# Optimization experiments

Hardware: AMD Instinct MI355X
Metric: run time of the kernel (lower is better)

Reference implementation:

```python
import jax, jax.numpy as jnp
import numpy as np
from math import lgamma, pi, sqrt

L = 20  # legendre_polys; embedding_dim = L*L = 400
SQ2 = sqrt(2.0)

def _norm(l, m):
    # K(l,m) = sqrt((2l+1)/(4pi) * (l-m)!/(l+m)!), computed stably via lgamma
    return sqrt((2 * l + 1) / (4.0 * pi)) * sqrt(np.exp(lgamma(l - m + 1) - lgamma(l + m + 1)))

def setup_inputs() -> dict:
    key = jax.random.key(0)
    k1, k2 = jax.random.split(key)
    B = 250000
    lon = jax.random.uniform(k1, (B,), minval=-180.0, maxval=180.0)
    lat = jax.random.uniform(k2, (B,), minval=-90.0, maxval=90.0)
    return {"lonlat": jnp.stack([lon, lat], axis=-1).astype(jnp.float32)}

def _sh_all(lonlat):
    # Real spherical harmonics for all (l, m), l in [0, L), m in [-l, l],
    # in the same ordering as the torch module's double loop.
    lon, lat = lonlat[:, 0], lonlat[:, 1]
    phi = jnp.deg2rad(lon + 180.0)    # azimuth in [0, 2pi)
    theta = jnp.deg2rad(lat + 90.0)   # colatitude in [0, pi]
    x = jnp.cos(theta)
    sx = jnp.sin(theta)               # = sqrt(1 - x^2) on [0, pi]

    # Associated Legendre P_l^m(x) (Condon-Shortley phase) via recurrence.
    P = {(0, 0): jnp.ones_like(x)}
    for m in range(1, L):
        P[(m, m)] = -(2 * m - 1) * sx * P[(m - 1, m - 1)]
    for m in range(L):
        if m + 1 < L:
            P[(m + 1, m)] = (2 * m + 1) * x * P[(m, m)]
        for l in range(m + 2, L):
            P[(l, m)] = ((2 * l - 1) * x * P[(l - 1, m)] - (l + m - 1) * P[(l - 2, m)]) / (l - m)

    cols = []
    for l in range(L):
        for m in range(-l, l + 1):
            am = abs(m)
            K = _norm(l, am)
            if m > 0:
                cols.append(SQ2 * K * jnp.cos(m * phi) * P[(l, m)])
            elif m < 0:
                cols.append(SQ2 * K * jnp.sin(am * phi) * P[(l, am)])
            else:
                cols.append(K * P[(l, 0)])
    return jnp.stack(cols, axis=-1)  # [B, L*L]

def reference(lonlat):
    return _sh_all(lonlat)
```

## Files before the change

kernel.cpp:

```cpp
#include <hip/hip_runtime.h>


#define L_MAX 20
#define NCOL 400
#define PTS 64
#define TPB 256
#define LSTR 205
#define SPLIT_L 14
#define C0A 0
#define CA 196
#define C0B 196
#define CB 204

constexpr double csqrt(double x) {
    double g = (x > 1.0) ? x : 1.0;
    for (int i = 0; i < 200; ++i) g = 0.5 * (g + x / g);
    return g;
}

struct CoefTbl { float c[NCOL]; };

constexpr CoefTbl make_tbl() {
    CoefTbl t{};
    const double PI  = 3.14159265358979323846;
    const double SQ2 = csqrt(2.0);
    for (int l = 0; l < L_MAX; ++l) {
        for (int m = 0; m <= l; ++m) {
            double r = 1.0;
            for (int k = l - m + 1; k <= l + m; ++k) r /= (double)k;
            double K = csqrt((2.0 * l + 1.0) / (4.0 * PI) * r);
            int base = l * l + l;
            if (m == 0) {
                t.c[base] = (float)K;
            } else {
                t.c[base + m] = (float)(SQ2 * K);
                t.c[base - m] = (float)(SQ2 * K);
            }
        }
    }
    return t;
}

static constexpr CoefTbl TBL = make_tbl();

__device__ constexpr int SUBOF[L_MAX] =
    {0,1,2,3, 3,2,1,0, 0,1,2,3, 3,2, 1,0,0,1, 2,3};

template<int L0, int L1, int C0>
__device__ __forceinline__ void sh_pass(int sub, float x, float sx,
                                        float c1, float s1,
                                        float* __restrict__ myrow) {
    constexpr int LTOP = L1 - 1;
    float pm = 1.0f;
    float cv = 1.0f, sv = 0.0f;

    auto emit = [&](int l, int m, float p) {
        if (l < L0) return;
        const int g = l * l + l;
        const int b = g - C0;
        if (m == 0) {
            myrow[b] = TBL.c[g] * p;
        } else {
            const float t = TBL.c[g + m] * p;
            myrow[b + m] = t * cv;
            myrow[b - m] = t * sv;
        }
    };

#pragma unroll
    for (int m = 0; m <= LTOP; ++m) {
        if (SUBOF[m] == sub) {
            float p2 = pm;
            emit(m, m, p2);
            if (m + 1 <= LTOP) {
                float p1 = float(2 * m + 1) * x * p2;
                emit(m + 1, m, p1);
#pragma unroll
                for (int l = m + 2; l <= LTOP; ++l) {
                    float p0 = (float(2 * l - 1) * x * p1 -
                                float(l + m - 1) * p2) *
                               (1.0f / float(l - m));
                    emit(l, m, p0);
                    p2 = p1; p1 = p0;
                }
            }
        }
        if (m < LTOP) {
            pm = -float(2 * m + 1) * sx * pm;
            float cn = cv * c1 - sv * s1;
            sv = sv * c1 + cv * s1;
            cv = cn;
        }
    }
}

template<int C0, int CW>
__device__ __forceinline__ void flush(const float* __restrict__ tile,
                                      float* __restrict__ outBase,
                                      int tid, int rem) {
    constexpr int G = CW / 4;
    constexpr int N = PTS * G;
    if (rem >= PTS) {
#pragma unroll 4
        for (int i = tid; i < N; i += TPB) {
            int pp = i / G;
            int cc = (i - pp * G) * 4;
            const float* s = tile + pp * LSTR + cc;
            float4 v = make_float4(s[0], s[1], s[2], s[3]);
            *reinterpret_cast<float4*>(outBase + pp * NCOL + C0 + cc) = v;
        }
    } else {
        for (int i = tid; i < N; i += TPB) {
            int pp = i / G;
            int cc = (i - pp * G) * 4;
            if (pp < rem) {
                const float* s = tile + pp * LSTR + cc;
                float4 v = make_float4(s[0], s[1], s[2], s[3]);
                *reinterpret_cast<float4*>(outBase + pp * NCOL + C0 + cc) = v;
            }
        }
    }
}

__global__ __launch_bounds__(TPB, 3) void sh_kernel(const float2* __restrict__ lonlat,
                                                    float* __restrict__ out, int B) {
    __shared__ float tile[PTS * LSTR];

    const int tid  = threadIdx.x;
    const int lane = tid & 63;
    const int sub  = tid >> 6;
    const int blockBase = blockIdx.x * PTS;
    const int rem = B - blockBase;
    const int p  = blockBase + lane;
    const int pr = p < B ? p : B - 1;

    float2 ll = lonlat[pr];
    const float D2R = 0.017453292519943295f;
    float phi   = (ll.x + 180.0f) * D2R;
    float theta = (ll.y + 90.0f) * D2R;

    float x, sx, s1, c1;
    sincosf(theta, &sx, &x);
    sincosf(phi, &s1, &c1);

    float* myrow = tile + lane * LSTR;
    float* outBase = out + (size_t)blockBase * NCOL;

    sh_pass<0, SPLIT_L, C0A>(sub, x, sx, c1, s1, myrow);

    __syncthreads();
    flush<C0A, CA>(tile, outBase, tid, rem);
    __syncthreads();

    sh_pass<SPLIT_L, L_MAX, C0B>(sub, x, sx, c1, s1, myrow);

    __syncthreads();
    flush<C0B, CB>(tile, outBase, tid, rem);
}

extern "C" void kernel_launch(void* const* d_in, const int* in_sizes, int n_in,
                              void* d_out, int out_size, void* d_ws, size_t ws_size,
                              hipStream_t stream) {
    (void)n_in; (void)d_ws; (void)ws_size; (void)out_size;
    const float2* lonlat = (const float2*)d_in[0];
    float* out = (float*)d_out;
    int B = in_sizes[0] / 2;

    const int blocks = (B + PTS - 1) / PTS;
    sh_kernel<<<blocks, TPB, 0, stream>>>(lonlat, out, B);
}
```

Measured before the change: 446.0 us.

## Double-buffer LDS tile across seven l-chunks, overlapping flush with compute

Restructures the kernel from two compute/flush phases into seven l-range chunks. Each chunk keeps its Legendre recurrence state in registers across chunks and writes into one of two smaller ping-pong LDS buffers, so one chunk's global store overlaps the next chunk's computation. It also replaces __syncthreads with a raw s_barrier plus an lgkmcnt wait, drops one barrier per stage, and raises the occupancy hint from 3 to 4. The cost is more barriers in total, more live registers for the per-m recurrence state, and narrower flush widths with more loop overhead.

Measured after the change: 463.5 us. +3.9%, slower.

```diff
diff --git a/kernel.cpp b/kernel.cpp
--- a/kernel.cpp
+++ b/kernel.cpp
@@ -5,12 +5,7 @@
 #define NCOL 400
 #define PTS 64
 #define TPB 256
-#define LSTR 205
-#define SPLIT_L 14
-#define C0A 0
-#define CA 196
-#define C0B 196
-#define CB 204
+#define LSTR 77
 
 constexpr double csqrt(double x) {
     double g = (x > 1.0) ? x : 1.0;
@@ -46,66 +41,61 @@
 __device__ constexpr int SUBOF[L_MAX] =
     {0,1,2,3, 3,2,1,0, 0,1,2,3, 3,2, 1,0,0,1, 2,3};
 
+#define BARRIER() do {                                      \
+    asm volatile("s_waitcnt lgkmcnt(0)" ::: "memory");      \
+    __builtin_amdgcn_s_barrier();                           \
+    asm volatile("" ::: "memory");                          \
+} while (0)
+
 template<int L0, int L1, int C0>
-__device__ __forceinline__ void sh_pass(int sub, float x, float sx,
-                                        float c1, float s1,
-                                        float* __restrict__ myrow) {
-    constexpr int LTOP = L1 - 1;
-    float pm = 1.0f;
-    float cv = 1.0f, sv = 0.0f;
-
-    auto emit = [&](int l, int m, float p) {
-        if (l < L0) return;
+__device__ __forceinline__ void computeChunk(int sub, float x,
+        float (&p1)[5], float (&p2)[5], const float (&pmmv)[5],
+        const float (&cmv)[5], const float (&smv)[5],
+        float* __restrict__ myrow) {
+#pragma unroll
+    for (int l = L0; l < L1; ++l) {
         const int g = l * l + l;
-        const int b = g - C0;
-        if (m == 0) {
-            myrow[b] = TBL.c[g] * p;
-        } else {
-            const float t = TBL.c[g + m] * p;
-            myrow[b + m] = t * cv;
-            myrow[b - m] = t * sv;
-        }
-    };
-
-#pragma unroll
-    for (int m = 0; m <= LTOP; ++m) {
-        if (SUBOF[m] == sub) {
-            float p2 = pm;
-            emit(m, m, p2);
-            if (m + 1 <= LTOP) {
-                float p1 = float(2 * m + 1) * x * p2;
-                emit(m + 1, m, p1);
-#pragma unroll
-                for (int l = m + 2; l <= LTOP; ++l) {
-                    float p0 = (float(2 * l - 1) * x * p1 -
-                                float(l + m - 1) * p2) *
-                               (1.0f / float(l - m));
-                    emit(l, m, p0);
-                    p2 = p1; p1 = p0;
-                }
-            }
-        }
-        if (m < LTOP) {
-            pm = -float(2 * m + 1) * sx * pm;
-            float cn = cv * c1 - sv * s1;
-            sv = sv * c1 + cv * s1;
-            cv = cn;
-        }
-    }
-}
-
-template<int C0, int CW>
-__device__ __forceinline__ void flush(const float* __restrict__ tile,
-                                      float* __restrict__ outBase,
-                                      int tid, int rem) {
-    constexpr int G = CW / 4;
+#pragma unroll
+        for (int m = 0; m <= l; ++m) {
+            if (SUBOF[m] != sub) continue;
+            const int s = m >> 2;
+            float pv;
+            if (l == m) {
+                pv = pmmv[s];
+                p1[s] = pv;
+            } else if (l == m + 1) {
+                pv = float(2 * m + 1) * x * p1[s];
+                p2[s] = p1[s];
+                p1[s] = pv;
+            } else {
+                pv = (float(2 * l - 1) * x * p1[s] -
+                      float(l + m - 1) * p2[s]) * (1.0f / float(l - m));
+                p2[s] = p1[s];
+                p1[s] = pv;
+            }
+            const int b = g - C0;
+            if (m == 0) {
+                myrow[b] = TBL.c[g] * pv;
+            } else {
+                const float t = TBL.c[g + m] * pv;
+                myrow[b + m] = t * cmv[s];
+                myrow[b - m] = t * smv[s];
+            }
+        }
+    }
+}
+
+template<int C0, int W>
+__device__ __forceinline__ void flushChunk(const float* __restrict__ src,
+                                           float* __restrict__ outBase,
+                                           int tid, int rem) {
+    constexpr int G = W / 4;
     constexpr int N = PTS * G;
     if (rem >= PTS) {
-#pragma unroll 4
         for (int i = tid; i < N; i += TPB) {
             int pp = i / G;
             int cc = (i - pp * G) * 4;
-            const float* s = tile + pp * LSTR + cc;
+            const float* s = src + pp * LSTR + cc;
             float4 v = make_float4(s[0], s[1], s[2], s[3]);
             *reinterpret_cast<float4*>(outBase + pp * NCOL + C0 + cc) = v;
         }
@@ -114,7 +104,7 @@
             int pp = i / G;
             int cc = (i - pp * G) * 4;
             if (pp < rem) {
-                const float* s = tile + pp * LSTR + cc;
+                const float* s = src + pp * LSTR + cc;
                 float4 v = make_float4(s[0], s[1], s[2], s[3]);
                 *reinterpret_cast<float4*>(outBase + pp * NCOL + C0 + cc) = v;
             }
@@ -122,9 +112,9 @@
     }
 }
 
-__global__ __launch_bounds__(TPB, 3) void sh_kernel(const float2* __restrict__ lonlat,
+__global__ __launch_bounds__(TPB, 4) void sh_kernel(const float2* __restrict__ lonlat,
                                                     float* __restrict__ out, int B) {
-    __shared__ float tile[PTS * LSTR];
+    __shared__ float tile[2][PTS * LSTR];
 
     const int tid  = threadIdx.x;
     const int lane = tid & 63;
@@ -143,19 +133,58 @@
     sincosf(theta, &sx, &x);
     sincosf(phi, &s1, &c1);
 
-    float* myrow = tile + lane * LSTR;
+    float p1[5], p2[5], pmmv[5], cmv[5], smv[5];
+#pragma unroll
+    for (int s = 0; s < 5; ++s) { p1[s]=0.f; p2[s]=0.f; pmmv[s]=0.f; cmv[s]=0.f; smv[s]=0.f; }
+    {
+        float pm = 1.0f, cv = 1.0f, sv = 0.0f;
+#pragma unroll
+        for (int m = 0; m < L_MAX; ++m) {
+            if (SUBOF[m] == sub) {
+                const int s = m >> 2;
+                pmmv[s] = pm; cmv[s] = cv; smv[s] = sv;
+            }
+            if (m < L_MAX - 1) {
+                pm = -float(2 * m + 1) * sx * pm;
+                float cn = cv * c1 - sv * s1;
+                sv = sv * c1 + cv * s1;
+                cv = cn;
+            }
+        }
+    }
+
+    float* row0 = &tile[0][lane * LSTR];
+    float* row1 = &tile[1][lane * LSTR];
     float* outBase = out + (size_t)blockBase * NCOL;
 
-    sh_pass<0, SPLIT_L, C0A>(sub, x, sx, c1, s1, myrow);
-
-    __syncthreads();
-    flush<C0A, CA>(tile, outBase, tid, rem);
-    __syncthreads();
-
-    sh_pass<SPLIT_L, L_MAX, C0B>(sub, x, sx, c1, s1, myrow);
-
-    __syncthreads();
-    flush<C0B, CB>(tile, outBase, tid, rem);
+    computeChunk<0, 6, 0>(sub, x, p1, p2, pmmv, cmv, smv, row0);
+    BARRIER();
+
+    flushChunk<0, 36>(tile[0], outBase, tid, rem);
+    computeChunk<6, 10, 36>(sub, x, p1, p2, pmmv, cmv, smv, row1);
+    BARRIER();
+
+    flushChunk<36, 64>(tile[1], outBase, tid, rem);
+    computeChunk<10, 12, 100>(sub, x, p1, p2, pmmv, cmv, smv, row0);
+    BARRIER();
+
+    flushChunk<100, 44>(tile[0], outBase, tid, rem);
+    computeChunk<12, 14, 144>(sub, x, p1, p2, pmmv, cmv, smv, row1);
+    BARRIER();
+
+    flushChunk<144, 52>(tile[1], outBase, tid, rem);
+    computeChunk<14, 16, 196>(sub, x, p1, p2, pmmv, cmv, smv, row0);
+    BARRIER();
+
+    flushChunk<196, 60>(tile[0], outBase, tid, rem);
+    computeChunk<16, 18, 256>(sub, x, p1, p2, pmmv, cmv, smv, row1);
+    BARRIER();
+
+    flushChunk<256, 68>(tile[1], outBase, tid, rem);
+    computeChunk<18, 20, 324>(sub, x, p1, p2, pmmv, cmv, smv, row0);
+    BARRIER();
+
+    flushChunk<324, 76>(tile[0], outBase, tid, rem);
 }
 
 extern "C" void kernel_launch(void* const* d_in, const int* in_sizes, int n_in,
```
